# Kernel tuning notes

Measured on AMD Instinct MI355X. Metric: run time of the kernel, lower is better.

Reference implementation:

```python
import jax, jax.numpy as jnp
import numpy as np

N_NODES = 50000
N_EDGES = 800000
HIDDEN = 256
N_LAYERS = 3
N_PAIRS = 4096


def setup_inputs() -> dict:
    key = jax.random.key(0)
    ks = jax.random.split(key, 10)
    s = 1.0 / np.sqrt(HIDDEN)
    x = jax.random.normal(ks[0], (N_NODES, HIDDEN), dtype=jnp.float32)
    f0_w = jax.random.normal(ks[1], (N_LAYERS, HIDDEN, HIDDEN), dtype=jnp.float32) * s
    f0_b = jax.random.normal(ks[2], (N_LAYERS, HIDDEN), dtype=jnp.float32) * s
    f1_w = jax.random.normal(ks[3], (N_LAYERS, HIDDEN, HIDDEN), dtype=jnp.float32) * s
    f1_b = jax.random.normal(ks[4], (N_LAYERS, HIDDEN), dtype=jnp.float32) * s
    conv_w = jax.random.normal(ks[5], (N_LAYERS, HIDDEN, HIDDEN), dtype=jnp.float32) * s
    conv_b = jax.random.normal(ks[6], (N_LAYERS, HIDDEN), dtype=jnp.float32) * s
    edge_src = jax.random.randint(ks[7], (N_EDGES,), 0, N_NODES, dtype=jnp.int64 if jax.config.jax_enable_x64 else jnp.int32)
    edge_dst = jax.random.randint(ks[8], (N_EDGES,), 0, N_NODES, dtype=edge_src.dtype)
    pos = jax.random.randint(ks[9], (N_PAIRS, 2), 0, N_NODES, dtype=edge_src.dtype)
    return {"x": x, "f0_w": f0_w, "f0_b": f0_b, "f1_w": f1_w, "f1_b": f1_b,
            "conv_w": conv_w, "conv_b": conv_b,
            "edge_src": edge_src, "edge_dst": edge_dst, "pos": pos}


def reference(x, f0_w, f0_b, f1_w, f1_b, conv_w, conv_b, edge_src, edge_dst, pos):
    # Faithful translation of FLabelingNet.forward:
    #   for each layer: x0 = f0(x); x0[idx] = f1(x[idx]); x = conv(x0, adj)
    #   return x[pos]
    n = x.shape[0]
    idx = pos.reshape(-1)  # (2M,) labeled node indices
    for i in range(f0_w.shape[0]):
        x0 = x @ f0_w[i] + f0_b[i]                       # (N, F) elementwise linear
        lbl = x[idx] @ f1_w[i] + f1_b[i]                 # (2M, F) transform of labeled rows
        x0 = x0.at[idx].set(lbl)                         # scatter-overwrite selected rows
        h = x0 @ conv_w[i] + conv_b[i]                   # node-wise linear of the conv
        # sparse adjacency message passing: out[v] = sum_{(u,v) in E} h[u]
        x = jax.ops.segment_sum(h[edge_src], edge_dst, num_segments=n)
    return x[pos]  # (M, 2, F)
```

## Files before the change

### kernel.cpp

```cpp
#include <hip/hip_runtime.h>
#include <hip/hip_bf16.h>

#define N_NODES 50000
#define N_EDGES 800000
#define HIDDEN  256
#define N_LAYERS 3
#define N_PAIRS 4096
#define N_LABEL 8192
#define NPAD    50176
#define SCAN_BLOCKS (NPAD / 256)
#define WSZ (HIDDEN * HIDDEN)

#define SLICE_ELEMS ((size_t)N_NODES * 32)
#define SEG_CHUNKS ((N_NODES + 63) / 64)

typedef __bf16 bf16x8 __attribute__((ext_vector_type(8)));
typedef __bf16 bf16x4 __attribute__((ext_vector_type(4)));
typedef float  f32x4  __attribute__((ext_vector_type(4)));

__device__ __forceinline__ void load_lds16(const void* g, void* l) {
    __builtin_amdgcn_global_load_lds(
        (const __attribute__((address_space(1))) void*)g,
        (__attribute__((address_space(3))) void*)l, 16, 0, 0);
}

template <bool DEG_BIAS, bool A_FP32>
__global__ __launch_bounds__(256) void mfma_gemm_fused(
    const void* __restrict__ A_in,
    const __bf16* __restrict__ Wt0, const __bf16* __restrict__ Wt1,
    const float* __restrict__ bD0, const float* __restrict__ bD1,
    const float* __restrict__ bC0, const float* __restrict__ bC1,
    __bf16* __restrict__ Cout,
    const int* __restrict__ idx,
    const int* __restrict__ offs,
    const int* __restrict__ flags,
    int M)
{
    const int role = blockIdx.z;
    if (role == 1 && blockIdx.x >= N_LABEL / 64) return;

    const __bf16* A   = (const __bf16*)A_in;
    const float*  A32 = (const float*)A_in;
    const __bf16* Wt  = role ? Wt1 : Wt0;
    const float*  bD  = role ? bD1 : bD0;
    const float*  bC  = role ? bC1 : bC0;

    __shared__ __bf16 As[64 * 32];
    __shared__ __bf16 Bs[128 * 32];
    __shared__ int s_idx[64];

    const int t    = threadIdx.x;
    const int lane = t & 63;
    const int wave = t >> 6;
    const int m0   = blockIdx.x * 64;
    const int n0   = blockIdx.y * 128;

    if (role == 1) {
        if (t < 64) s_idx[t] = idx[m0 + t];
        __syncthreads();
    }

    const int arow  = t >> 2;
    const int acol8 = (t & 3) * 8;
    int anode;
    if (role == 1) {
        anode = s_idx[arow];
    } else {
        const int rg = m0 + arow;
        anode = (rg < M) ? rg : (M - 1);
    }
    const __bf16* aptr   = A   + (size_t)anode * HIDDEN + acol8;
    const float*  aptr32 = A32 + (size_t)anode * HIDDEN + acol8;

    const __bf16* bptr[2];
    #pragma unroll
    for (int r = 0; r < 2; ++r) {
        const int c = r * 256 + t;
        bptr[r] = Wt + (size_t)(n0 + (c >> 2)) * HIDDEN + (c & 3) * 8;
    }

    f32x4 acc[8];
    #pragma unroll
    for (int i = 0; i < 8; ++i) acc[i] = (f32x4){0.f, 0.f, 0.f, 0.f};

    const int wm   = wave * 16;
    const int fm   = lane & 15;
    const int quad = lane >> 4;

    for (int k0 = 0; k0 < HIDDEN; k0 += 32) {
        __syncthreads();
        if constexpr (A_FP32) {
            const float* ap = aptr32 + k0;
            const float4 u0 = *(const float4*)(ap);
            const float4 u1 = *(const float4*)(ap + 4);
            bf16x8 w = {(__bf16)u0.x, (__bf16)u0.y, (__bf16)u0.z, (__bf16)u0.w,
                        (__bf16)u1.x, (__bf16)u1.y, (__bf16)u1.z, (__bf16)u1.w};
            *(bf16x8*)(As + (size_t)t * 8) = w;
        } else {
            load_lds16(aptr + k0, (void*)(As + (size_t)t * 8));
        }
        #pragma unroll
        for (int r = 0; r < 2; ++r)
            load_lds16(bptr[r] + k0, (void*)(Bs + (size_t)(r * 256 + t) * 8));
        __syncthreads();

        const bf16x8 af = *(const bf16x8*)(As + (wm + fm) * 32 + quad * 8);
        bf16x8 bfr[8];
        #pragma unroll
        for (int nt = 0; nt < 8; ++nt)
            bfr[nt] = *(const bf16x8*)(Bs + (nt * 16 + fm) * 32 + quad * 8);

        #pragma unroll
        for (int nt = 0; nt < 8; ++nt)
            acc[nt] = __builtin_amdgcn_mfma_f32_16x16x32_bf16(
                af, bfr[nt], acc[nt], 0, 0, 0);
    }

    float bd[8], bc[8];
    #pragma unroll
    for (int nt = 0; nt < 8; ++nt) {
        const int col = n0 + nt * 16 + fm;
        bd[nt] = DEG_BIAS ? bD[col] : 0.f;
        bc[nt] = bC[col];
    }

    #pragma unroll
    for (int rg = 0; rg < 4; ++rg) {
        const int rloc = wm + quad * 4 + rg;
        int orow;
        if (role == 1) {
            orow = s_idx[rloc];
        } else {
            orow = m0 + rloc;
            if (orow >= M) continue;
            if (flags[orow]) continue;
        }
        float bscale = 0.f;
        if constexpr (DEG_BIAS)
            bscale = (float)(offs[orow + 1] - offs[orow]);
        #pragma unroll
        for (int nt = 0; nt < 8; ++nt) {
            const int cb = n0 + nt * 16;
            float v = acc[nt][rg];
            if constexpr (DEG_BIAS) v += bscale * bd[nt];
            v += bc[nt];
            Cout[(size_t)(cb >> 5) * SLICE_ELEMS + (size_t)orow * 32
                 + (cb & 31) + fm] = (__bf16)v;
        }
    }
}

template <bool GATHER_A, bool DEG_BIAS, bool DEG_VIA_IDX, bool OUT_BF16, bool PROD_BATCH>
__global__ __launch_bounds__(256) void mfma_gemm(
    const __bf16* __restrict__ A_in,
    const __bf16* __restrict__ Wt_in,
    const float* __restrict__ biasD,
    void* __restrict__ Cout_in,
    const int* __restrict__ idx,
    const int* __restrict__ offs,
    int M)
{
    const __bf16* A  = A_in;
    const __bf16* Wt = Wt_in;
    void* Cout = Cout_in;
    if constexpr (PROD_BATCH) {
        const int z = blockIdx.z;
        A    = A_in  + (size_t)(3 * (1 + (z >> 1)) + (z & 1)) * WSZ;
        Wt   = Wt_in + (size_t)(z >> 1) * WSZ;
        Cout = (void*)((__bf16*)Cout_in + (size_t)z * WSZ);
    }

    __shared__ __bf16 As[64 * 32];
    __shared__ __bf16 Bs[128 * 32];
    __shared__ int s_idx[64];

    const int t    = threadIdx.x;
    const int lane = t & 63;
    const int wave = t >> 6;
    const int m0   = blockIdx.x * 64;
    const int n0   = blockIdx.y * 128;

    if constexpr (GATHER_A || DEG_VIA_IDX) {
        if (t < 64) s_idx[t] = idx[m0 + t];
        __syncthreads();
    }

    const int arow  = t >> 2;
    const int acol8 = (t & 3) * 8;
    int anode;
    if constexpr (GATHER_A) {
        anode = s_idx[arow];
    } else {
        const int rg = m0 + arow;
        anode = (rg < M) ? rg : (M - 1);
    }
    const __bf16* aptr = A + (size_t)anode * HIDDEN + acol8;

    const __bf16* bptr[2];
    #pragma unroll
    for (int r = 0; r < 2; ++r) {
        const int c = r * 256 + t;
        bptr[r] = Wt + (size_t)(n0 + (c >> 2)) * HIDDEN + (c & 3) * 8;
    }

    f32x4 acc[8];
    #pragma unroll
    for (int i = 0; i < 8; ++i) acc[i] = (f32x4){0.f, 0.f, 0.f, 0.f};

    const int wm   = wave * 16;
    const int fm   = lane & 15;
    const int quad = lane >> 4;

    for (int k0 = 0; k0 < HIDDEN; k0 += 32) {
        __syncthreads();
        load_lds16(aptr + k0, (void*)(As + (size_t)t * 8));
        #pragma unroll
        for (int r = 0; r < 2; ++r)
            load_lds16(bptr[r] + k0, (void*)(Bs + (size_t)(r * 256 + t) * 8));
        __syncthreads();

        const bf16x8 af = *(const bf16x8*)(As + (wm + fm) * 32 + quad * 8);
        bf16x8 bfr[8];
        #pragma unroll
        for (int nt = 0; nt < 8; ++nt)
            bfr[nt] = *(const bf16x8*)(Bs + (nt * 16 + fm) * 32 + quad * 8);

        #pragma unroll
        for (int nt = 0; nt < 8; ++nt)
            acc[nt] = __builtin_amdgcn_mfma_f32_16x16x32_bf16(
                af, bfr[nt], acc[nt], 0, 0, 0);
    }

    float bd[8];
    #pragma unroll
    for (int nt = 0; nt < 8; ++nt)
        bd[nt] = DEG_BIAS ? biasD[n0 + nt * 16 + fm] : 0.f;

    #pragma unroll
    for (int rg = 0; rg < 4; ++rg) {
        const int rloc = wm + quad * 4 + rg;
        const int orow = m0 + rloc;
        if (!PROD_BATCH && orow >= M) continue;
        int dnode = orow;
        if constexpr (GATHER_A || DEG_VIA_IDX) dnode = s_idx[rloc];
        float bscale = 0.f;
        if constexpr (DEG_BIAS)
            bscale = (float)(offs[dnode + 1] - offs[dnode]);
        #pragma unroll
        for (int nt = 0; nt < 8; ++nt) {
            const int col = n0 + nt * 16 + fm;
            float v = acc[nt][rg];
            if constexpr (DEG_BIAS) v += bscale * bd[nt];
            if constexpr (OUT_BF16)
                ((__bf16*)Cout)[(size_t)orow * HIDDEN + col] = (__bf16)v;
            else
                ((float*)Cout)[(size_t)orow * HIDDEN + col] = v;
        }
    }
}

__global__ __launch_bounds__(256) void wconv_kernel(
    const float* __restrict__ f0_w, const float* __restrict__ f1_w,
    const float* __restrict__ conv_w, const float* __restrict__ conv_b,
    __bf16* __restrict__ wt_all, __bf16* __restrict__ cw_nt,
    float* __restrict__ q)
{
    const int z = blockIdx.z;
    const int kx = blockIdx.x * 32, nx = blockIdx.y * 32;
    const int tx = threadIdx.x, ty = threadIdx.y;

    if (z < 9) {
        const int layer = z / 3, which = z % 3;
        const float* W = ((which == 0) ? f0_w : (which == 1) ? f1_w : conv_w)
                         + (size_t)layer * WSZ;
        __bf16* T = wt_all + (size_t)z * WSZ;

        __shared__ float tile[32][33];
        for (int i = ty; i < 32; i += 8)
            tile[i][tx] = W[(size_t)(kx + i) * HIDDEN + nx + tx];
        __syncthreads();
        for (int i = ty; i < 32; i += 8)
            T[(size_t)(nx + i) * HIDDEN + kx + tx] = (__bf16)tile[tx][i];
    } else if (z < 11) {
        const int layer = z - 9;
        const float* W = conv_w + (size_t)layer * WSZ;
        __bf16* T = cw_nt + (size_t)layer * WSZ;
        for (int i = ty; i < 32; i += 8)
            T[(size_t)(kx + i) * HIDDEN + nx + tx] =
                (__bf16)W[(size_t)(kx + i) * HIDDEN + nx + tx];
    } else {
        if (blockIdx.x >= 4 || blockIdx.y != 0) return;
        const int zq = blockIdx.x;
        const int l = zq >> 1, branch = zq & 1;
        const float* cb = conv_b + (size_t)l * HIDDEN;
        const float* W  = (branch ? f1_w : f0_w) + (size_t)(l + 1) * WSZ;
        const int n = ty * 32 + tx;
        float s = 0.f;
        #pragma unroll 4
        for (int k = 0; k < HIDDEN; ++k)
            s += cb[k] * W[(size_t)k * HIDDEN + n];
        q[(size_t)zq * HIDDEN + n] = s;
    }
}

__global__ __launch_bounds__(256) void hist_kernel(
    const int* __restrict__ dst, const int* __restrict__ pos,
    int* __restrict__ counts, int* __restrict__ flags)
{
    int e = blockIdx.x * 256 + threadIdx.x;
    if (e < N_EDGES) atomicAdd(&counts[dst[e]], 1);
    if (e < N_LABEL) flags[pos[e]] = 1;
}

__device__ __forceinline__ int block_incl_scan(int v, int* s, int t)
{
    s[t] = v; __syncthreads();
    #pragma unroll
    for (int off = 1; off < 256; off <<= 1) {
        int add = (t >= off) ? s[t - off] : 0;
        __syncthreads();
        s[t] += add;
        __syncthreads();
    }
    return s[t];
}

__global__ __launch_bounds__(256) void scan1_kernel(
    const int* __restrict__ counts, int* __restrict__ offs, int* __restrict__ bsum)
{
    __shared__ int s[256];
    const int t = threadIdx.x;
    const int i = blockIdx.x * 256 + t;
    const int v = counts[i];
    int incl = block_incl_scan(v, s, t);
    offs[i] = incl - v;
    if (t == 255) bsum[blockIdx.x] = incl;
}

__global__ __launch_bounds__(256) void scan2_kernel(
    const int* __restrict__ bsum, int* __restrict__ bbase)
{
    __shared__ int s[256];
    const int t = threadIdx.x;
    const int v = (t < SCAN_BLOCKS) ? bsum[t] : 0;
    int incl = block_incl_scan(v, s, t);
    bbase[t] = incl - v;
}

__global__ __launch_bounds__(256) void scan3_kernel(
    int* __restrict__ offs, const int* __restrict__ bbase, int* __restrict__ cursor)
{
    const int i = blockIdx.x * 256 + threadIdx.x;
    const int o = offs[i] + bbase[blockIdx.x];
    offs[i] = o;
    cursor[i] = o;
}

__global__ __launch_bounds__(256) void fill_kernel(
    const int* __restrict__ src, const int* __restrict__ dst,
    int* __restrict__ cursor, int* __restrict__ src_sorted)
{
    int e = blockIdx.x * 256 + threadIdx.x;
    if (e < N_EDGES) {
        int p = atomicAdd(&cursor[dst[e]], 1);
        src_sorted[p] = src[e];
    }
}

template <bool COMPACT>
__global__ __launch_bounds__(256) void seg_slice_kernel(
    const __bf16* __restrict__ x0b,
    const int* __restrict__ srcs,
    const int* __restrict__ offs,
    const int* __restrict__ nodelist,
    __bf16* __restrict__ out)
{
    const int slice = blockIdx.x & 7;
    const int chunk = blockIdx.x >> 3;
    const int t    = threadIdx.x;
    const int wave = t >> 6;
    const int lane = t & 63;
    const int g    = lane >> 2;
    const int li   = lane & 3;
    const int rw   = chunk * 64 + wave * 16 + g;
    if (!COMPACT && rw >= N_NODES) return;

    const int d   = COMPACT ? nodelist[rw] : rw;
    const int beg = offs[d];
    const int deg = offs[d + 1] - beg;

    const __bf16* xs = x0b + (size_t)slice * SLICE_ELEMS + li * 8;

    float a[8];
    #pragma unroll
    for (int q = 0; q < 8; ++q) a[q] = 0.f;

    int vs = (li < deg) ? srcs[beg + li] : 0;
    for (int base = 0; base < deg; base += 4) {
        const int rem = deg - base;
        const int n   = rem < 4 ? rem : 4;
        const int nb  = base + 4;
        int vs_n = 0;
        if (nb + li < deg) vs_n = srcs[beg + nb + li];

        int ss[4];
        #pragma unroll
        for (int k = 0; k < 4; ++k) ss[k] = __shfl(vs, (g << 2) + k);
        bf16x8 c[4];
        #pragma unroll
        for (int k = 0; k < 4; ++k)
            if (k < n) c[k] = *(const bf16x8*)(xs + (size_t)ss[k] * 32);
        #pragma unroll
        for (int k = 0; k < 4; ++k) {
            if (k < n) {
                #pragma unroll
                for (int q = 0; q < 8; ++q) a[q] += (float)c[k][q];
            }
        }
        vs = vs_n;
    }

    bf16x8 o;
    #pragma unroll
    for (int q = 0; q < 8; ++q) o[q] = (__bf16)a[q];
    *(bf16x8*)(out + (size_t)rw * HIDDEN + (slice << 5) + li * 8) = o;
}

extern "C" void kernel_launch(void* const* d_in, const int* in_sizes, int n_in,
                              void* d_out, int out_size, void* d_ws, size_t ws_size,
                              hipStream_t stream)
{
    const float* x       = (const float*)d_in[0];
    const float* f0_w    = (const float*)d_in[1];
    const float* f0_b    = (const float*)d_in[2];
    const float* f1_w    = (const float*)d_in[3];
    const float* f1_b    = (const float*)d_in[4];
    const float* conv_w  = (const float*)d_in[5];
    const float* conv_b  = (const float*)d_in[6];
    const int*   edge_src = (const int*)d_in[7];
    const int*   edge_dst = (const int*)d_in[8];
    const int*   pos      = (const int*)d_in[9];
    float* out = (float*)d_out;

    const size_t buf = (size_t)N_NODES * HIDDEN;

    char* p = (char*)d_ws;
    __bf16* bufA   = (__bf16*)p; p += buf * 2;
    __bf16* bufB   = (__bf16*)p; p += buf * 2;
    __bf16* s_lbl  = (__bf16*)p; p += (size_t)N_LABEL * HIDDEN * 2;
    __bf16* wt_all = (__bf16*)p; p += (size_t)9 * WSZ * 2;
    __bf16* prod   = (__bf16*)p; p += (size_t)4 * WSZ * 2;
    __bf16* cw_nt  = (__bf16*)p; p += (size_t)2 * WSZ * 2;
    float*  qv     = (float*)p;  p += (size_t)4 * HIDDEN * 4;
    int* counts     = (int*)p;  p += NPAD * 4;
    int* flags      = (int*)p;  p += NPAD * 4;
    int* offs       = (int*)p;  p += NPAD * 4;
    int* bsum       = (int*)p;  p += 256 * 4;
    int* bbase      = (int*)p;  p += 256 * 4;
    int* src_sorted = (int*)p;  p += (size_t)N_EDGES * 4;
    int* cursor = counts;

    const int edge_blocks = (N_EDGES + 255) / 256;

    hipMemsetAsync(counts, 0, 2 * NPAD * sizeof(int), stream);
    hist_kernel<<<edge_blocks, 256, 0, stream>>>(edge_dst, pos, counts, flags);
    scan1_kernel<<<SCAN_BLOCKS, 256, 0, stream>>>(counts, offs, bsum);
    scan2_kernel<<<1, 256, 0, stream>>>(bsum, bbase);
    scan3_kernel<<<SCAN_BLOCKS, 256, 0, stream>>>(offs, bbase, cursor);
    fill_kernel<<<edge_blocks, 256, 0, stream>>>(edge_src, edge_dst, cursor, src_sorted);

    wconv_kernel<<<dim3(8, 8, 12), dim3(32, 8), 0, stream>>>(
        f0_w, f1_w, conv_w, conv_b, wt_all, cw_nt, qv);

    mfma_gemm<false, false, false, true, true><<<dim3(4, 2, 4), 256, 0, stream>>>(
        wt_all, cw_nt, nullptr, prod, nullptr, nullptr, HIDDEN);

    const dim3 fused_grid(782, 2, 2);
    const dim3 lbl_grid(128, 2);

    __bf16* cur = bufA;
    __bf16* tmp = bufB;

    for (int l = 0; l < N_LAYERS; ++l) {
        const float* B0 = f0_b + (size_t)l * HIDDEN;
        const float* B1 = f1_b + (size_t)l * HIDDEN;

        if (l == 0) {
            mfma_gemm_fused<false, true><<<fused_grid, 256, 0, stream>>>(
                x, wt_all + 0 * WSZ, wt_all + 1 * WSZ,
                nullptr, nullptr, B0, B1, tmp, pos, offs, flags, N_NODES);
        } else {
            const int z0 = (l - 1) * 2;
            mfma_gemm_fused<true, false><<<fused_grid, 256, 0, stream>>>(
                cur, prod + (size_t)z0 * WSZ, prod + (size_t)(z0 + 1) * WSZ,
                qv + (size_t)z0 * HIDDEN, qv + (size_t)(z0 + 1) * HIDDEN,
                B0, B1, tmp, pos, offs, flags, N_NODES);
        }

        if (l < N_LAYERS - 1) {
            seg_slice_kernel<false><<<8 * SEG_CHUNKS, 256, 0, stream>>>(
                tmp, src_sorted, offs, nullptr, cur);
        } else {
            seg_slice_kernel<true><<<8 * (N_LABEL / 64), 256, 0, stream>>>(
                tmp, src_sorted, offs, pos, s_lbl);
            mfma_gemm<false, true, true, false, false><<<lbl_grid, 256, 0, stream>>>(
                s_lbl, wt_all + (size_t)(2 * 3 + 2) * WSZ,
                conv_b + (size_t)2 * HIDDEN, out, pos, offs, N_LABEL);
        }
    }
}
```

Measured before the change: 399.1 us.

## Pad CSR segments to multiples of eight with zero-row sentinel for branchless gather

Pads each node's edge list in the CSR to a multiple of 8, filling the extra slots with a sentinel index that points to an added all-zero row in each feature slice. The segment-sum kernel can then load 8 neighbor indices with two int4 reads and issue 8 unconditional 16-byte gathers per iteration, accumulating with bit-shift bf16-to-fp32 conversion. Degree for the bias term now comes from the kept counts array, because offsets now include padding. This removes per-element bounds checks and shuffles in the gather loop, at the cost of extra wasted loads on padding (about 3.5 per node on average) and a larger index array.

```diff
diff --git a/kernel.cpp b/kernel.cpp
--- a/kernel.cpp
+++ b/kernel.cpp
@@ -11,17 +11,26 @@
 #define SCAN_BLOCKS (NPAD / 256)
 #define WSZ (HIDDEN * HIDDEN)
 
-#define SLICE_ELEMS ((size_t)N_NODES * 32)
+#define NROWPAD (N_NODES + 1)
+#define SLICE_ELEMS ((size_t)NROWPAD * 32)
 #define SEG_CHUNKS ((N_NODES + 63) / 64)
 
 typedef __bf16 bf16x8 __attribute__((ext_vector_type(8)));
 typedef __bf16 bf16x4 __attribute__((ext_vector_type(4)));
 typedef float  f32x4  __attribute__((ext_vector_type(4)));
+typedef float  f32x2  __attribute__((ext_vector_type(2)));
 
 __device__ __forceinline__ void load_lds16(const void* g, void* l) {
     __builtin_amdgcn_global_load_lds(
         (const __attribute__((address_space(1))) void*)g,
         (__attribute__((address_space(3))) void*)l, 16, 0, 0);
+}
+
+__device__ __forceinline__ void acc8(const uint4 w, f32x2* a) {
+    a[0] += (f32x2){__uint_as_float(w.x << 16), __uint_as_float(w.x & 0xffff0000u)};
+    a[1] += (f32x2){__uint_as_float(w.y << 16), __uint_as_float(w.y & 0xffff0000u)};
+    a[2] += (f32x2){__uint_as_float(w.z << 16), __uint_as_float(w.z & 0xffff0000u)};
+    a[3] += (f32x2){__uint_as_float(w.w << 16), __uint_as_float(w.w & 0xffff0000u)};
 }
 
 template <bool DEG_BIAS, bool A_FP32>
@@ -32,7 +41,7 @@
     const float* __restrict__ bC0, const float* __restrict__ bC1,
     __bf16* __restrict__ Cout,
     const int* __restrict__ idx,
-    const int* __restrict__ offs,
+    const int* __restrict__ degv,
     const int* __restrict__ flags,
     int M)
 {
@@ -137,7 +146,7 @@
         }
         float bscale = 0.f;
         if constexpr (DEG_BIAS)
-            bscale = (float)(offs[orow + 1] - offs[orow]);
+            bscale = (float)degv[orow];
         #pragma unroll
         for (int nt = 0; nt < 8; ++nt) {
             const int cb = n0 + nt * 16;
@@ -157,7 +166,7 @@
     const float* __restrict__ biasD,
     void* __restrict__ Cout_in,
     const int* __restrict__ idx,
-    const int* __restrict__ offs,
+    const int* __restrict__ degv,
     int M)
 {
     const __bf16* A  = A_in;
@@ -245,7 +254,7 @@
         if constexpr (GATHER_A || DEG_VIA_IDX) dnode = s_idx[rloc];
         float bscale = 0.f;
         if constexpr (DEG_BIAS)
-            bscale = (float)(offs[dnode + 1] - offs[dnode]);
+            bscale = (float)degv[dnode];
         #pragma unroll
         for (int nt = 0; nt < 8; ++nt) {
             const int col = n0 + nt * 16 + fm;
@@ -305,11 +314,16 @@
 
 __global__ __launch_bounds__(256) void hist_kernel(
     const int* __restrict__ dst, const int* __restrict__ pos,
-    int* __restrict__ counts, int* __restrict__ flags)
+    int* __restrict__ counts, int* __restrict__ flags,
+    __bf16* __restrict__ x0b)
 {
     int e = blockIdx.x * 256 + threadIdx.x;
     if (e < N_EDGES) atomicAdd(&counts[dst[e]], 1);
     if (e < N_LABEL) flags[pos[e]] = 1;
+    if (blockIdx.x == 0) {
+        const int sl = threadIdx.x >> 5, c = threadIdx.x & 31;
+        x0b[(size_t)sl * SLICE_ELEMS + (size_t)N_NODES * 32 + c] = (__bf16)0.f;
+    }
 }
 
 __device__ __forceinline__ int block_incl_scan(int v, int* s, int t)
@@ -331,9 +345,9 @@
     __shared__ int s[256];
     const int t = threadIdx.x;
     const int i = blockIdx.x * 256 + t;
-    const int v = counts[i];
-    int incl = block_incl_scan(v, s, t);
-    offs[i] = incl - v;
+    const int pv = (counts[i] + 7) & ~7;
+    int incl = block_incl_scan(pv, s, t);
+    offs[i] = incl - pv;
     if (t == 255) bsum[blockIdx.x] = incl;
 }
 
@@ -348,12 +362,17 @@
 }
 
 __global__ __launch_bounds__(256) void scan3_kernel(
-    int* __restrict__ offs, const int* __restrict__ bbase, int* __restrict__ cursor)
+    int* __restrict__ offs, const int* __restrict__ bbase,
+    int* __restrict__ cursor, const int* __restrict__ counts,
+    int* __restrict__ src_sorted)
 {
     const int i = blockIdx.x * 256 + threadIdx.x;
     const int o = offs[i] + bbase[blockIdx.x];
     offs[i] = o;
     cursor[i] = o;
+    const int v  = counts[i];
+    const int pv = (v + 7) & ~7;
+    for (int j = o + v; j < o + pv; ++j) src_sorted[j] = N_NODES;
 }
 
 __global__ __launch_bounds__(256) void fill_kernel(
@@ -385,44 +404,48 @@
     const int rw   = chunk * 64 + wave * 16 + g;
     if (!COMPACT && rw >= N_NODES) return;
 
-    const int d   = COMPACT ? nodelist[rw] : rw;
-    const int beg = offs[d];
-    const int deg = offs[d + 1] - beg;
-
-    const __bf16* xs = x0b + (size_t)slice * SLICE_ELEMS + li * 8;
-
-    float a[8];
-    #pragma unroll
-    for (int q = 0; q < 8; ++q) a[q] = 0.f;
-
-    int vs = (li < deg) ? srcs[beg + li] : 0;
-    for (int base = 0; base < deg; base += 4) {
-        const int rem = deg - base;
-        const int n   = rem < 4 ? rem : 4;
-        const int nb  = base + 4;
-        int vs_n = 0;
-        if (nb + li < deg) vs_n = srcs[beg + nb + li];
-
-        int ss[4];
-        #pragma unroll
-        for (int k = 0; k < 4; ++k) ss[k] = __shfl(vs, (g << 2) + k);
-        bf16x8 c[4];
-        #pragma unroll
-        for (int k = 0; k < 4; ++k)
-            if (k < n) c[k] = *(const bf16x8*)(xs + (size_t)ss[k] * 32);
-        #pragma unroll
-        for (int k = 0; k < 4; ++k) {
-            if (k < n) {
-                #pragma unroll
-                for (int q = 0; q < 8; ++q) a[q] += (float)c[k][q];
-            }
-        }
-        vs = vs_n;
+    const int d    = COMPACT ? nodelist[rw] : rw;
+    const int beg  = offs[d];
+    const int pdeg = offs[d + 1] - beg;
+
+    const char* xb = (const char*)(x0b + (size_t)slice * SLICE_ELEMS);
+    const uint32_t lioff = (uint32_t)li * 16u;
+    const int* sp = srcs + beg;
+
+    f32x2 a[4];
+    #pragma unroll
+    for (int j = 0; j < 4; ++j) a[j] = (f32x2){0.f, 0.f};
+
+    int4 j0, j1;
+    if (pdeg > 0) {
+        j0 = *(const int4*)(sp);
+        j1 = *(const int4*)(sp + 4);
+    }
+
+    for (int base = 0; base < pdeg; base += 8) {
+        const int4 k0 = j0, k1 = j1;
+        if (base + 8 < pdeg) {
+            j0 = *(const int4*)(sp + base + 8);
+            j1 = *(const int4*)(sp + base + 12);
+        }
+        const uint4 c0 = *(const uint4*)(xb + (((uint32_t)k0.x << 6) + lioff));
+        const uint4 c1 = *(const uint4*)(xb + (((uint32_t)k0.y << 6) + lioff));
+        const uint4 c2 = *(const uint4*)(xb + (((uint32_t)k0.z << 6) + lioff));
+        const uint4 c3 = *(const uint4*)(xb + (((uint32_t)k0.w << 6) + lioff));
+        const uint4 c4 = *(const uint4*)(xb + (((uint32_t)k1.x << 6) + lioff));
+        const uint4 c5 = *(const uint4*)(xb + (((uint32_t)k1.y << 6) + lioff));
+        const uint4 c6 = *(const uint4*)(xb + (((uint32_t)k1.z << 6) + lioff));
+        const uint4 c7 = *(const uint4*)(xb + (((uint32_t)k1.w << 6) + lioff));
+        acc8(c0, a); acc8(c1, a); acc8(c2, a); acc8(c3, a);
+        acc8(c4, a); acc8(c5, a); acc8(c6, a); acc8(c7, a);
     }
 
     bf16x8 o;
     #pragma unroll
-    for (int q = 0; q < 8; ++q) o[q] = (__bf16)a[q];
+    for (int j = 0; j < 4; ++j) {
+        o[2 * j]     = (__bf16)a[j].x;
+        o[2 * j + 1] = (__bf16)a[j].y;
+    }
     *(bf16x8*)(out + (size_t)rw * HIDDEN + (slice << 5) + li * 8) = o;
 }
 
@@ -446,7 +469,7 @@
 
     char* p = (char*)d_ws;
     __bf16* bufA   = (__bf16*)p; p += buf * 2;
-    __bf16* bufB   = (__bf16*)p; p += buf * 2;
+    __bf16* bufB   = (__bf16*)p; p += SLICE_ELEMS * 8 * 2;
     __bf16* s_lbl  = (__bf16*)p; p += (size_t)N_LABEL * HIDDEN * 2;
     __bf16* wt_all = (__bf16*)p; p += (size_t)9 * WSZ * 2;
     __bf16* prod   = (__bf16*)p; p += (size_t)4 * WSZ * 2;
@@ -455,18 +478,18 @@
     int* counts     = (int*)p;  p += NPAD * 4;
     int* flags      = (int*)p;  p += NPAD * 4;
     int* offs       = (int*)p;  p += NPAD * 4;
+    int* cursor     = (int*)p;  p += NPAD * 4;
     int* bsum       = (int*)p;  p += 256 * 4;
     int* bbase      = (int*)p;  p += 256 * 4;
-    int* src_sorted = (int*)p;  p += (size_t)N_EDGES * 4;
-    int* cursor = counts;
+    int* src_sorted = (int*)p;  p += (size_t)(N_EDGES + 7 * NPAD) * 4;
 
     const int edge_blocks = (N_EDGES + 255) / 256;
 
     hipMemsetAsync(counts, 0, 2 * NPAD * sizeof(int), stream);
-    hist_kernel<<<edge_blocks, 256, 0, stream>>>(edge_dst, pos, counts, flags);
+    hist_kernel<<<edge_blocks, 256, 0, stream>>>(edge_dst, pos, counts, flags, bufB);
     scan1_kernel<<<SCAN_BLOCKS, 256, 0, stream>>>(counts, offs, bsum);
     scan2_kernel<<<1, 256, 0, stream>>>(bsum, bbase);
-    scan3_kernel<<<SCAN_BLOCKS, 256, 0, stream>>>(offs, bbase, cursor);
+    scan3_kernel<<<SCAN_BLOCKS, 256, 0, stream>>>(offs, bbase, cursor, counts, src_sorted);
     fill_kernel<<<edge_blocks, 256, 0, stream>>>(edge_src, edge_dst, cursor, src_sorted);
 
     wconv_kernel<<<dim3(8, 8, 12), dim3(32, 8), 0, stream>>>(
@@ -488,13 +511,13 @@
         if (l == 0) {
             mfma_gemm_fused<false, true><<<fused_grid, 256, 0, stream>>>(
                 x, wt_all + 0 * WSZ, wt_all + 1 * WSZ,
-                nullptr, nullptr, B0, B1, tmp, pos, offs, flags, N_NODES);
+                nullptr, nullptr, B0, B1, tmp, pos, counts, flags, N_NODES);
         } else {
             const int z0 = (l - 1) * 2;
             mfma_gemm_fused<true, false><<<fused_grid, 256, 0, stream>>>(
                 cur, prod + (size_t)z0 * WSZ, prod + (size_t)(z0 + 1) * WSZ,
                 qv + (size_t)z0 * HIDDEN, qv + (size_t)(z0 + 1) * HIDDEN,
-                B0, B1, tmp, pos, offs, flags, N_NODES);
+                B0, B1, tmp, pos, counts, flags, N_NODES);
         }
 
         if (l < N_LAYERS - 1) {
@@ -505,7 +528,7 @@
                 tmp, src_sorted, offs, pos, s_lbl);
             mfma_gemm<false, true, true, false, false><<<lbl_grid, 256, 0, stream>>>(
                 s_lbl, wt_all + (size_t)(2 * 3 + 2) * WSZ,
-                conv_b + (size_t)2 * HIDDEN, out, pos, offs, N_LABEL);
-        }
-    }
-}
+                conv_b + (size_t)2 * HIDDEN, out, pos, counts, N_LABEL);
+        }
+    }
+}
```

Result: faster. 389.5 us (-2.4%).
